# Kernel optimization log

Measured on AMD Instinct MI355X. Metric: run time of the kernel, lower is better.

Reference implementation:

```python
import jax, jax.numpy as jnp
import numpy as np

N_GRAPHS = 32   # number of graphs (equal-size contiguous segments in `batch`)
SEG_LEN = 512   # nodes per graph
NUM_HEADS = 16
LN_EPS = 1e-5


def setup_inputs() -> dict:
    key = jax.random.key(0)
    ks = jax.random.split(key, 4)
    N = N_GRAPHS * SEG_LEN
    D = 1024
    x = jax.random.normal(ks[0], (N, D), dtype=jnp.float32)
    # contiguous equal-size graph segments (what per-graph batching produces)
    batch = jnp.repeat(jnp.arange(N_GRAPHS, dtype=jnp.int64), SEG_LEN)
    s = 1.0 / np.sqrt(D)
    w_in = jax.random.normal(ks[1], (3 * D, D), dtype=jnp.float32) * s
    b_in = jnp.zeros((3 * D,), dtype=jnp.float32)
    w_out = jax.random.normal(ks[2], (D, D), dtype=jnp.float32) * s
    b_out = jnp.zeros((D,), dtype=jnp.float32)
    gamma = jnp.ones((D,), dtype=jnp.float32)
    beta = jnp.zeros((D,), dtype=jnp.float32)
    return {"x": x, "batch": batch, "w_in": w_in, "b_in": b_in,
            "w_out": w_out, "b_out": b_out, "gamma": gamma, "beta": beta}


def _mha_blockdiag(x, w_in, b_in, w_out, b_out):
    # Packed per-graph self-attention: identical math to looping MHA over each
    # graph's node subset, but done in one dense batched attention.
    N, D = x.shape
    G, S, H = N_GRAPHS, SEG_LEN, NUM_HEADS
    dh = D // H
    qkv = x @ w_in.T + b_in                       # (N, 3D)
    qkv = qkv.reshape(G, S, 3, H, dh)
    q, k, v = qkv[:, :, 0], qkv[:, :, 1], qkv[:, :, 2]  # (G, S, H, dh)
    scale = 1.0 / jnp.sqrt(jnp.asarray(dh, x.dtype))
    scores = jnp.einsum('gqhd,gkhd->ghqk', q, k) * scale  # (G, H, S, S)
    probs = jax.nn.softmax(scores, axis=-1)
    ctx = jnp.einsum('ghqk,gkhd->gqhd', probs, v).reshape(N, D)
    return ctx @ w_out.T + b_out


def reference(x, batch, w_in, b_in, w_out, b_out, gamma, beta):
    attn_out = _mha_blockdiag(x, w_in, b_in, w_out, b_out)
    # dropout is identity in eval mode; residual + LayerNorm
    h = x + attn_out
    mu = jnp.mean(h, axis=-1, keepdims=True)
    var = jnp.var(h, axis=-1, keepdims=True)
    return (h - mu) * jax.lax.rsqrt(var + LN_EPS) * gamma + beta
```

## Files before the change

### kernel.cpp

```cpp
#include <hip/hip_runtime.h>
#include <hip/hip_bf16.h>
#include <math.h>

#define N_TOK  16384
#define DMODEL 1024
#define GRAPHS 32
#define SEGLEN 512
#define HEADS  16
#define DH     64
#define D3     3072
#define QK_LD  2048
#define KDIM   1024
#define NT_K   16

typedef __bf16 bf16;
typedef __attribute__((ext_vector_type(4))) __bf16 bf16x4;
typedef __attribute__((ext_vector_type(8))) __bf16 bf16x8;
typedef __attribute__((ext_vector_type(4))) float f32x4;

#define N4_X  (N_TOK * DMODEL / 4)
#define N4_WI (D3 * DMODEL / 4)
#define N4_WO (DMODEL * DMODEL / 4)
__global__ __launch_bounds__(256) void cvt_all(const float* __restrict__ x,
                                               const float* __restrict__ w_in,
                                               const float* __restrict__ w_out,
                                               bf16* __restrict__ xb,
                                               bf16* __restrict__ wb,
                                               bf16* __restrict__ wob) {
    int i = blockIdx.x * blockDim.x + threadIdx.x;
    const float* src; bf16* dst; int j;
    if (i < N4_X)                { src = x;     dst = xb;  j = i; }
    else if (i < N4_X + N4_WI)   { src = w_in;  dst = wb;  j = i - N4_X; }
    else                         { src = w_out; dst = wob; j = i - N4_X - N4_WI; }
    float4 v = ((const float4*)src)[j];
    bf16x4 o;
    o[0] = (bf16)v.x; o[1] = (bf16)v.y; o[2] = (bf16)v.z; o[3] = (bf16)v.w;
    ((bf16x4*)dst)[j] = o;
}

template<int EPI, int VSPLIT>
__global__ __launch_bounds__(256, 3) void gemm128(
    const bf16* __restrict__ A, const bf16* __restrict__ B,
    const float* __restrict__ bias, const float* __restrict__ resid,
    void* __restrict__ C, bf16* __restrict__ vT, int N, int nbn, int ldc)
{
    __shared__ bf16x8 smA[1024];
    __shared__ bf16x8 smB[1024];
    const int tid  = threadIdx.x;
    const int lane = tid & 63, w = tid >> 6;
    const int wr = w >> 1, wc = w & 1;
    const int l15 = lane & 15, l4 = lane >> 4;
    const int r7 = l15 & 7;

    const int nwg = (int)gridDim.x;
    const int bid = (int)blockIdx.x;
    const int sw  = (bid & 7) * (nwg >> 3) + (bid >> 3);
    const int bm0 = (sw / nbn) * 128, bn0 = (sw % nbn) * 128;

    const int srow = tid >> 3, skb = tid & 7;

    uint4 pa[4], pb[4];
    auto PF_LOAD = [&](int t) {
        const int k0 = t * 64;
        #pragma unroll
        for (int q = 0; q < 4; q++) {
            int row = q * 32 + srow;
            pa[q] = *(const uint4*)(A + (size_t)(bm0 + row) * KDIM + k0 + skb * 8);
            pb[q] = *(const uint4*)(B + (size_t)(bn0 + row) * KDIM + k0 + skb * 8);
        }
    };
    auto LDS_WRITE = [&]() {
        #pragma unroll
        for (int q = 0; q < 4; q++) {
            int row = q * 32 + srow;
            smA[row * 8 + (skb ^ (row & 7))] = __builtin_bit_cast(bf16x8, pa[q]);
            smB[row * 8 + (skb ^ (row & 7))] = __builtin_bit_cast(bf16x8, pb[q]);
        }
    };

    f32x4 acc[4][4] = {};

    PF_LOAD(0);
    LDS_WRITE();
    __syncthreads();

    #pragma unroll 1
    for (int t = 0; t < NT_K; ++t) {
        if (t + 1 < NT_K) PF_LOAD(t + 1);
        #pragma unroll
        for (int kp = 0; kp < 2; kp++) {
            const int slot = kp * 4 + l4;
            bf16x8 af[4], bfr[4];
            #pragma unroll
            for (int m = 0; m < 4; m++)
                af[m] = smA[(wr * 64 + m * 16 + l15) * 8 + (slot ^ r7)];
            #pragma unroll
            for (int n = 0; n < 4; n++)
                bfr[n] = smB[(wc * 64 + n * 16 + l15) * 8 + (slot ^ r7)];
            #pragma unroll
            for (int m = 0; m < 4; m++)
                #pragma unroll
                for (int n = 0; n < 4; n++)
                    acc[m][n] = __builtin_amdgcn_mfma_f32_16x16x32_bf16(af[m], bfr[n], acc[m][n], 0, 0, 0);
        }
        __syncthreads();
        if (t + 1 < NT_K) {
            LDS_WRITE();
            __syncthreads();
        }
    }

    #pragma unroll
    for (int m = 0; m < 4; m++) {
        #pragma unroll
        for (int n = 0; n < 4; n++) {
            const int col  = bn0 + wc * 64 + n * 16 + l15;
            const int row0 = bm0 + wr * 64 + m * 16 + l4 * 4;
            const float bv = bias[col];
            if (EPI == 1) {
                #pragma unroll
                for (int i = 0; i < 4; i++) {
                    float v = acc[m][n][i] + bv + resid[(size_t)(row0 + i) * N + col];
                    ((bf16*)C)[(size_t)(row0 + i) * ldc + col] = (bf16)v;
                }
            } else if (VSPLIT && bn0 >= 2048) {
                const int cc = col - 2048;
                bf16x4 pk;
                #pragma unroll
                for (int i = 0; i < 4; i++) pk[i] = (bf16)(acc[m][n][i] + bv);
                *(bf16x4*)(vT + ((size_t)((row0 >> 9) * HEADS + (cc >> 6)) * DH + (cc & 63)) * SEGLEN
                               + (row0 & (SEGLEN - 1))) = pk;
            } else {
                const float sc = (VSPLIT && bn0 < 1024) ? 0.125f : 1.0f;
                #pragma unroll
                for (int i = 0; i < 4; i++)
                    ((bf16*)C)[(size_t)(row0 + i) * ldc + col] = (bf16)((acc[m][n][i] + bv) * sc);
            }
        }
    }
}

__global__ __launch_bounds__(256) void attn_kernel(
    const bf16* __restrict__ qkA, const bf16* __restrict__ vT, bf16* __restrict__ ctx)
{
    const int qt = blockIdx.x, h = blockIdx.y, g = blockIdx.z;
    __shared__ bf16 smP[128 * 64];
    const int tid = threadIdx.x, lane = tid & 63, w = tid >> 6;
    const int l15 = lane & 15, l4 = lane >> 4;
    const int r7 = l15 & 7;
    const int grow0 = g * SEGLEN, qbase = qt * 128;
    const bf16* kbase = qkA + (size_t)grow0 * QK_LD + 1024 + h * 64 + (size_t)l4 * 8;
    const bf16* vbase = vT + (size_t)(g * HEADS + h) * DH * SEGLEN + (size_t)l4 * 8;

    bf16x8 qf[2][2];
    #pragma unroll
    for (int m = 0; m < 2; m++)
        #pragma unroll
        for (int kp = 0; kp < 2; kp++)
            qf[m][kp] = *(const bf16x8*)(qkA + (size_t)(grow0 + qbase + w * 32 + m * 16 + l15) * QK_LD
                                          + h * 64 + (kp * 4 + l4) * 8);

    f32x4 acc[2][4] = {};
    float mrow[2][4], lrow[2][4];
    #pragma unroll
    for (int m = 0; m < 2; m++)
        #pragma unroll
        for (int i = 0; i < 4; i++) { mrow[m][i] = -INFINITY; lrow[m][i] = 0.f; }

    #pragma unroll 2
    for (int t = 0; t < 8; t++) {
        f32x4 s[2][4] = {};
        #pragma unroll
        for (int kp = 0; kp < 2; kp++) {
            #pragma unroll
            for (int n = 0; n < 4; n++) {
                bf16x8 kf = *(const bf16x8*)(kbase + (size_t)(t * 64 + n * 16 + l15) * QK_LD + kp * 32);
                #pragma unroll
                for (int m = 0; m < 2; m++)
                    s[m][n] = __builtin_amdgcn_mfma_f32_16x16x32_bf16(qf[m][kp], kf, s[m][n], 0, 0, 0);
            }
        }
        float mx[2][4];
        int need = 0;
        #pragma unroll
        for (int m = 0; m < 2; m++)
            #pragma unroll
            for (int i = 0; i < 4; i++) {
                float m0 = fmaxf(fmaxf(s[m][0][i], s[m][1][i]), fmaxf(s[m][2][i], s[m][3][i]));
                #pragma unroll
                for (int d = 1; d < 16; d <<= 1) m0 = fmaxf(m0, __shfl_xor(m0, d));
                mx[m][i] = m0;
                need |= (m0 > mrow[m][i] + 8.0f) ? 1 : 0;
            }
        if (__any(need)) {
            #pragma unroll
            for (int m = 0; m < 2; m++)
                #pragma unroll
                for (int i = 0; i < 4; i++) {
                    float mn = fmaxf(mrow[m][i], mx[m][i]);
                    float alpha = __expf(mrow[m][i] - mn);
                    mrow[m][i] = mn;
                    lrow[m][i] *= alpha;
                    #pragma unroll
                    for (int n = 0; n < 4; n++) acc[m][n][i] *= alpha;
                }
        }
        float rsum[2][4] = {};
        #pragma unroll
        for (int m = 0; m < 2; m++)
            #pragma unroll
            for (int n = 0; n < 4; n++)
                #pragma unroll
                for (int i = 0; i < 4; i++) {
                    float p = __expf(s[m][n][i] - mrow[m][i]);
                    rsum[m][i] += p;
                    int prow = w * 32 + m * 16 + l4 * 4 + i;
                    smP[prow * 64 + ((n * 16 + l15) ^ ((prow & 7) << 3))] = (bf16)p;
                }
        #pragma unroll
        for (int m = 0; m < 2; m++)
            #pragma unroll
            for (int i = 0; i < 4; i++) {
                #pragma unroll
                for (int d = 1; d < 16; d <<= 1) rsum[m][i] += __shfl_xor(rsum[m][i], d);
                lrow[m][i] += rsum[m][i];
            }
        #pragma unroll
        for (int kp = 0; kp < 2; kp++) {
            bf16x8 pf[2];
            #pragma unroll
            for (int m = 0; m < 2; m++)
                pf[m] = ((const bf16x8*)smP)[(w * 32 + m * 16 + l15) * 8 + ((kp * 4 + l4) ^ r7)];
            #pragma unroll
            for (int n = 0; n < 4; n++) {
                bf16x8 vf = *(const bf16x8*)(vbase + (size_t)(n * 16 + l15) * SEGLEN + t * 64 + kp * 32);
                #pragma unroll
                for (int m = 0; m < 2; m++)
                    acc[m][n] = __builtin_amdgcn_mfma_f32_16x16x32_bf16(pf[m], vf, acc[m][n], 0, 0, 0);
            }
        }
    }

    #pragma unroll
    for (int m = 0; m < 2; m++)
        #pragma unroll
        for (int i = 0; i < 4; i++) {
            float inv = 1.f / lrow[m][i];
            int row = grow0 + qbase + w * 32 + m * 16 + l4 * 4 + i;
            #pragma unroll
            for (int n = 0; n < 4; n++) {
                int col = h * 64 + n * 16 + l15;
                ctx[(size_t)row * DMODEL + col] = (bf16)(acc[m][n][i] * inv);
            }
        }
}

__global__ __launch_bounds__(256) void ln_kernel(
    const bf16* __restrict__ h, const float* __restrict__ gamma,
    const float* __restrict__ beta, float* __restrict__ out)
{
    const int row = blockIdx.x;
    bf16x4 hv = ((const bf16x4*)(h + (size_t)row * DMODEL))[threadIdx.x];
    float v0 = (float)hv[0], v1 = (float)hv[1], v2 = (float)hv[2], v3 = (float)hv[3];
    float s  = v0 + v1 + v2 + v3;
    float ss = v0 * v0 + v1 * v1 + v2 * v2 + v3 * v3;
    #pragma unroll
    for (int d = 1; d < 64; d <<= 1) { s += __shfl_xor(s, d); ss += __shfl_xor(ss, d); }
    __shared__ float red[8];
    int wv = threadIdx.x >> 6, lane = threadIdx.x & 63;
    if (lane == 0) { red[wv] = s; red[4 + wv] = ss; }
    __syncthreads();
    s  = red[0] + red[1] + red[2] + red[3];
    ss = red[4] + red[5] + red[6] + red[7];
    float mu  = s * (1.f / 1024.f);
    float var = ss * (1.f / 1024.f) - mu * mu;
    float rs  = rsqrtf(var + 1e-5f);
    float4 gv = ((const float4*)gamma)[threadIdx.x];
    float4 bv = ((const float4*)beta)[threadIdx.x];
    float4 o;
    o.x = (v0 - mu) * rs * gv.x + bv.x;
    o.y = (v1 - mu) * rs * gv.y + bv.y;
    o.z = (v2 - mu) * rs * gv.z + bv.z;
    o.w = (v3 - mu) * rs * gv.w + bv.w;
    ((float4*)(out + (size_t)row * DMODEL))[threadIdx.x] = o;
}

extern "C" void kernel_launch(void* const* d_in, const int* in_sizes, int n_in,
                              void* d_out, int out_size, void* d_ws, size_t ws_size,
                              hipStream_t stream) {
    const float* x     = (const float*)d_in[0];
    const float* w_in  = (const float*)d_in[2];
    const float* b_in  = (const float*)d_in[3];
    const float* w_out = (const float*)d_in[4];
    const float* b_out = (const float*)d_in[5];
    const float* gamma = (const float*)d_in[6];
    const float* beta  = (const float*)d_in[7];
    float* out = (float*)d_out;

    char* ws = (char*)d_ws;
    bf16*  xb   = (bf16*)ws;
    bf16*  wb   = (bf16*)(ws + 33554432);
    bf16*  wob  = (bf16*)(ws + 39845888);
    bf16*  qkA  = (bf16*)(ws + 41943040);
    bf16*  vT   = (bf16*)(ws + 109051904);
    bf16*  ctxb = xb;
    bf16*  hbuf = qkA;

    cvt_all<<<(N4_X + N4_WI + N4_WO) / 256, 256, 0, stream>>>(x, w_in, w_out, xb, wb, wob);

    gemm128<0, 1><<<3072, 256, 0, stream>>>(xb, wb, b_in, nullptr, qkA, vT,
                                            D3, 24, QK_LD);
    attn_kernel<<<dim3(4, 16, 32), 256, 0, stream>>>(qkA, vT, ctxb);

    gemm128<1, 0><<<1024, 256, 0, stream>>>(ctxb, wob, b_out, x, hbuf, nullptr,
                                            DMODEL, 8, DMODEL);
    ln_kernel<<<N_TOK, 256, 0, stream>>>(hbuf, gamma, beta, out);
}
```

Measured before the change: 339.4 us.

## Stage K/V tiles in shared memory with register prefetch; remap GEMM tile order

The attention kernel now loads each 64-row K and V tile cooperatively into double-buffered, XOR-swizzled shared memory, prefetching the next tile into registers while computing on the current one. Previously each wave read K and V fragments directly from global memory, so the four waves fetched the same data redundantly. The GEMM block-index swizzle is also changed to group blocks into 8-column-tile groups, aiming for better L2 reuse. The cost is more shared memory and registers in the attention kernel, a full unroll of its t loop, and an extra barrier per tile.

Measured after the change: 308.3 us. 1.1x faster.

```diff
diff --git a/kernel.cpp b/kernel.cpp
--- a/kernel.cpp
+++ b/kernel.cpp
@@ -52,10 +52,16 @@
     const int l15 = lane & 15, l4 = lane >> 4;
     const int r7 = l15 & 7;
 
-    const int nwg = (int)gridDim.x;
-    const int bid = (int)blockIdx.x;
-    const int sw  = (bid & 7) * (nwg >> 3) + (bid >> 3);
-    const int bm0 = (sw / nbn) * 128, bn0 = (sw % nbn) * 128;
+    const int nwg  = (int)gridDim.x;
+    const int x    = (int)blockIdx.x & 7;
+    const int c    = (int)blockIdx.x >> 3;
+    const int nmtx = (nwg >> 3) / nbn;
+    const int gsz  = nmtx * 8;
+    const int grp  = c / gsz;
+    const int rem  = c - grp * gsz;
+    const int mt   = x * nmtx + (rem >> 3);
+    const int nt   = grp * 8 + (rem & 7);
+    const int bm0  = mt * 128, bn0 = nt * 128;
 
     const int srow = tid >> 3, skb = tid & 7;
 
@@ -144,13 +150,14 @@
     const bf16* __restrict__ qkA, const bf16* __restrict__ vT, bf16* __restrict__ ctx)
 {
     const int qt = blockIdx.x, h = blockIdx.y, g = blockIdx.z;
+    __shared__ bf16x8 smK[2][64 * 8];
+    __shared__ bf16x8 smV[2][64 * 8];
     __shared__ bf16 smP[128 * 64];
     const int tid = threadIdx.x, lane = tid & 63, w = tid >> 6;
     const int l15 = lane & 15, l4 = lane >> 4;
     const int r7 = l15 & 7;
     const int grow0 = g * SEGLEN, qbase = qt * 128;
-    const bf16* kbase = qkA + (size_t)grow0 * QK_LD + 1024 + h * 64 + (size_t)l4 * 8;
-    const bf16* vbase = vT + (size_t)(g * HEADS + h) * DH * SEGLEN + (size_t)l4 * 8;
+    const size_t vbase = (size_t)(g * HEADS + h) * DH * SEGLEN;
 
     bf16x8 qf[2][2];
     #pragma unroll
@@ -167,14 +174,35 @@
         #pragma unroll
         for (int i = 0; i < 4; i++) { mrow[m][i] = -INFINITY; lrow[m][i] = 0.f; }
 
-    #pragma unroll 2
+    uint4 kr[2][2], vr[2][2];
+    auto LOADT = [&](int t, int dst) {
+        #pragma unroll
+        for (int q = 0; q < 2; q++) {
+            int c = tid + 256 * q, r = c >> 3, cb = c & 7;
+            kr[dst][q] = *(const uint4*)(qkA + (size_t)(grow0 + t * 64 + r) * QK_LD + 1024 + h * 64 + cb * 8);
+            vr[dst][q] = *(const uint4*)(vT + vbase + (size_t)r * SEGLEN + t * 64 + cb * 8);
+        }
+    };
+    LOADT(0, 0);
+
+    #pragma unroll
     for (int t = 0; t < 8; t++) {
+        const int cur = t & 1;
+        #pragma unroll
+        for (int q = 0; q < 2; q++) {
+            int c = tid + 256 * q, r = c >> 3, cb = c & 7;
+            smK[cur][r * 8 + (cb ^ (r & 7))] = __builtin_bit_cast(bf16x8, kr[cur][q]);
+            smV[cur][r * 8 + (cb ^ (r & 7))] = __builtin_bit_cast(bf16x8, vr[cur][q]);
+        }
+        if (t < 7) LOADT(t + 1, cur ^ 1);
+        __syncthreads();
+
         f32x4 s[2][4] = {};
         #pragma unroll
         for (int kp = 0; kp < 2; kp++) {
             #pragma unroll
             for (int n = 0; n < 4; n++) {
-                bf16x8 kf = *(const bf16x8*)(kbase + (size_t)(t * 64 + n * 16 + l15) * QK_LD + kp * 32);
+                bf16x8 kf = smK[cur][(n * 16 + l15) * 8 + ((kp * 4 + l4) ^ r7)];
                 #pragma unroll
                 for (int m = 0; m < 2; m++)
                     s[m][n] = __builtin_amdgcn_mfma_f32_16x16x32_bf16(qf[m][kp], kf, s[m][n], 0, 0, 0);
@@ -233,7 +261,7 @@
                 pf[m] = ((const bf16x8*)smP)[(w * 32 + m * 16 + l15) * 8 + ((kp * 4 + l4) ^ r7)];
             #pragma unroll
             for (int n = 0; n < 4; n++) {
-                bf16x8 vf = *(const bf16x8*)(vbase + (size_t)(n * 16 + l15) * SEGLEN + t * 64 + kp * 32);
+                bf16x8 vf = smV[cur][(n * 16 + l15) * 8 + ((kp * 4 + l4) ^ r7)];
                 #pragma unroll
                 for (int m = 0; m < 2; m++)
                     acc[m][n] = __builtin_amdgcn_mfma_f32_16x16x32_bf16(pf[m], vf, acc[m][n], 0, 0, 0);
```
